# Optimization experiments

Measured on AMD Instinct MI355X. Metric: run time of the kernel, lower is better.

Reference implementation:

```python
import jax, jax.numpy as jnp
import numpy as np

H = 1024   # hidden_dim
C = 56     # numchars
T = 64     # total_timesteps


def setup_inputs() -> dict:
    key = jax.random.key(0)
    ks = jax.random.split(key, 20)

    def p(k, shape, fan_in):
        # torch default Linear/LSTM init: U(-1/sqrt(fan), 1/sqrt(fan))
        return jax.random.uniform(k, shape, jnp.float32, -1.0, 1.0) / np.float32(np.sqrt(fan_in))

    return {
        "input_sentence": jax.random.normal(ks[0], (T, C), jnp.float32),
        # ErrorUnit.W per layer (top-layer ErrorUnit is never run)
        "W0_w": p(ks[1], (H, C), C), "W0_b": p(ks[2], (H,), C),
        "W1_w": p(ks[3], (H, H), H), "W1_b": p(ks[4], (H,), H),
        "W2_w": p(ks[5], (H, H), H), "W2_b": p(ks[6], (H,), H),
        # LSTM input weights; h0=c0=0 every call so W_hh is inert; b = b_ih + b_hh
        "Wih1": p(ks[7], (4 * H, 2 * H), H), "b1": p(ks[8], (4 * H,), H),
        "Wih2": p(ks[9], (4 * H, 2 * H), H), "b2": p(ks[10], (4 * H,), H),
        "Wih3": p(ks[11], (4 * H, H), H), "b3": p(ks[12], (4 * H,), H),
        # StateUnit.V (reconstruction) per layer >= 1; layer0's V is never used
        "V1_w": p(ks[13], (C, H), H), "V1_b": p(ks[14], (C,), H),
        "V2_w": p(ks[15], (H, H), H), "V2_b": p(ks[16], (H,), H),
        "V3_w": p(ks[17], (H, H), H), "V3_b": p(ks[18], (H,), H),
        "iternumber": 500,
    }


def _lstm_out(x, Wih, b):
    # nn.LSTM(seq=1, batch=1) with zero initial state: f-gate dead, h = o*tanh(i*g)
    z = Wih @ x + b
    i, _, g, o = jnp.split(z, 4)
    return jax.nn.sigmoid(o) * jnp.tanh(jax.nn.sigmoid(i) * jnp.tanh(g))


def reference(input_sentence, W0_w, W0_b, W1_w, W1_b, W2_w, W2_b,
              Wih1, b1, Wih2, b2, Wih3, b3,
              V1_w, V1_b, V2_w, V2_b, V3_w, V3_b, iternumber):
    lam = 1e-4 if iternumber <= 1000 else 1e-2  # lambda1 / lambda2 branch
    h, c = W0_w.shape

    def step(carry, x_t):
        # TD1, TD2: previous-timestep TD errors (fed to LSTM inputs)
        # recon1..3: previous-timestep reconstructions from the layer above
        TD1, TD2, recon1, recon2, recon3, loss = carry
        # layer 0: state is clamped to the input char
        nTD0 = x_t - recon1                        # [C]
        BU0 = W0_w @ nTD0 + W0_b                   # [H]
        loss = loss + jnp.sum(jnp.abs(nTD0))       # * lam**0
        # layer 1
        s1 = _lstm_out(jnp.concatenate([BU0, TD1]), Wih1, b1)
        nrecon1 = V1_w @ s1 + V1_b                 # [C]
        nTD1 = s1 - recon2
        BU1 = W1_w @ nTD1 + W1_b
        loss = loss + jnp.sum(jnp.abs(nTD1)) * lam
        # layer 2
        s2 = _lstm_out(jnp.concatenate([BU1, TD2]), Wih2, b2)
        nrecon2 = V2_w @ s2 + V2_b
        nTD2 = s2 - recon3
        BU2 = W2_w @ nTD2 + W2_b
        loss = loss + jnp.sum(jnp.abs(nTD2)) * (lam ** 2)
        # layer 3 (top): ErrorUnit never runs, its TD_err stays zero -> zero loss term
        s3 = _lstm_out(BU2, Wih3, b3)
        nrecon3 = V3_w @ s3 + V3_b
        return (nTD1, nTD2, nrecon1, nrecon2, nrecon3, loss), None

    z = lambda n: jnp.zeros((n,), jnp.float32)
    init = (z(h), z(h), z(c), z(h), z(h), jnp.float32(0.0))
    carry, _ = jax.lax.scan(step, init, input_sentence)
    return carry[-1]
```

## Files before the change

kernel.cpp:

```cpp
#include <hip/hip_runtime.h>

#define CC 56
#define TT 64
#define GRID 1024
#define NT 256
#define NFLAG 64
#define SS 32
#define FB (GRID * SS)
#define AGENT __HIP_MEMORY_SCOPE_AGENT

#define OFF_FWS   147456
#define OFF_W1BF  262144
#define OFF_W2BF  2359296
#define OFF_PRIV  4456448
#define PRIVB     32768

#define PM2  0
#define PM3  3072
#define PW1R 6144
#define PW2R 9216
#define PV2  12288
#define PV3  13312
#define PV1  14336
#define PA0  15360

#define FS1   0
#define FS2   1024
#define FS3   2048
#define FTD1  3072
#define FTD2  5120
#define FRC1  7168

static __device__ __forceinline__ float wredsum(float v) {
#pragma unroll
  for (int m = 32; m; m >>= 1) v += __shfl_xor(v, m, 64);
  return v;
}
static __device__ __forceinline__ float sigm(float x) { return 1.f / (1.f + __expf(-x)); }
static __device__ __forceinline__ float ftanh(float x) {
  x = fminf(15.f, fmaxf(-15.f, x));
  float e = __expf(2.f * x);
  return (e - 1.f) / (e + 1.f);
}

static __device__ __forceinline__ float2 cld2(const float* p) {
  unsigned long long u = __hip_atomic_load((const unsigned long long*)p, __ATOMIC_RELAXED, AGENT);
  union { unsigned long long u; float2 f; } c; c.u = u; return c.f;
}
static __device__ __forceinline__ float4 cld4(const float* p) {
  float2 a = cld2(p), b = cld2(p + 2);
  return make_float4(a.x, a.y, b.x, b.y);
}
static __device__ __forceinline__ float cld1(const float* p) {
  return __uint_as_float(__hip_atomic_load((const unsigned int*)p, __ATOMIC_RELAXED, AGENT));
}
static __device__ __forceinline__ void cst1(float* p, float v) {
  __hip_atomic_store((unsigned int*)p, __float_as_uint(v), __ATOMIC_RELAXED, AGENT);
}
static __device__ __forceinline__ void cstu2(unsigned* p, unsigned a, unsigned b) {
  unsigned long long u = (unsigned long long)a | ((unsigned long long)b << 32);
  __hip_atomic_store((unsigned long long*)p, u, __ATOMIC_RELAXED, AGENT);
}
static __device__ __forceinline__ int ldi(const int* p) {
  return __hip_atomic_load(p, __ATOMIC_RELAXED, AGENT);
}
static __device__ __forceinline__ void sti(int* p, int v) {
  __hip_atomic_store(p, v, __ATOMIC_RELAXED, AGENT);
}

static __device__ __forceinline__ unsigned bfp(float lo, float hi) {
  unsigned a = __float_as_uint(lo), b = __float_as_uint(hi);
  a = (a + 0x7fffu + ((a >> 16) & 1u)) >> 16;
  b = (b + 0x7fffu + ((b >> 16) & 1u)) >> 16;
  return a | (b << 16);
}
static __device__ __forceinline__ float blo(unsigned u) { return __uint_as_float(u << 16); }
static __device__ __forceinline__ float bhi(unsigned u) { return __uint_as_float(u & 0xffff0000u); }
static __device__ __forceinline__ float bdot2(uint2 w, float4 v) {
  float r = blo(w.x) * v.x;
  r = fmaf(bhi(w.x), v.y, r);
  r = fmaf(blo(w.y), v.z, r);
  r = fmaf(bhi(w.y), v.w, r);
  return r;
}

static __device__ __forceinline__ void warr(int* iws, int g, int b) {
  __syncthreads();
  if (threadIdx.x == 0) sti(iws + SS * b, g);
}
static __device__ __forceinline__ void wwait(int* iws, int g, int b) {
  if (b == 0) {
    const int* p0 = iws + SS * threadIdx.x;
    for (;;) {
      int a0 = ldi(p0), a1 = ldi(p0 + SS * 256), a2 = ldi(p0 + SS * 512), a3 = ldi(p0 + SS * 768);
      if (a0 >= g && a1 >= g && a2 >= g && a3 >= g) break;
      __builtin_amdgcn_s_sleep(1);
    }
    __syncthreads();
    if (threadIdx.x < NFLAG) sti(iws + FB + SS * threadIdx.x, g);
  } else {
    if (threadIdx.x == 0)
      while (ldi(iws + FB + SS * (b & (NFLAG - 1))) < g) __builtin_amdgcn_s_sleep(1);
  }
  __asm__ __volatile__("" ::: "memory");
  __syncthreads();
}

static __device__ __forceinline__ float dotw(const float* a, const float* c, int lane) {
  const float4* a4 = (const float4*)a;
  const float4* c4 = (const float4*)c;
  float acc = 0.f;
#pragma unroll
  for (int j = 0; j < 4; ++j) {
    float4 x = a4[lane * 4 + j], y = c4[lane * 4 + j];
    acc = fmaf(x.x, y.x, fmaf(x.y, y.y, fmaf(x.z, y.z, fmaf(x.w, y.w, acc))));
  }
  return wredsum(acc);
}

__global__ void __launch_bounds__(NT, 4) predcells(
    const float* __restrict__ inp,
    const float* __restrict__ W0w, const float* __restrict__ W0b,
    const float* __restrict__ W1w, const float* __restrict__ W1b,
    const float* __restrict__ W2w, const float* __restrict__ W2b,
    const float* __restrict__ Wi1, const float* __restrict__ b1,
    const float* __restrict__ Wi2, const float* __restrict__ b2,
    const float* __restrict__ Wi3, const float* __restrict__ b3,
    const float* __restrict__ V1w, const float* __restrict__ V1b,
    const float* __restrict__ V2w, const float* __restrict__ V2b,
    const float* __restrict__ V3w, const float* __restrict__ V3b,
    const int* __restrict__ itn,
    float* __restrict__ out, char* ws)
{
  const int tid = threadIdx.x;
  const int lane = tid & 63;
  const int wv = tid >> 6;
  const int b = blockIdx.x;
  const bool hasV1 = (b < CC);

  int* iws = (int*)ws;
  float* fws = (float*)(ws + OFF_FWS);
  unsigned short* w1bf = (unsigned short*)(ws + OFF_W1BF);
  unsigned short* w2bf = (unsigned short*)(ws + OFF_W2BF);
  unsigned short* priv = (unsigned short*)(ws + OFF_PRIV + (size_t)b * PRIVB);

  __shared__ float arow[6][1024];
  __shared__ float psX[6][4], psP[3][4], psA[3];
  __shared__ float cs1[3], cs2[3], cs3[3];

  const int gofs = (wv == 0) ? 0 : ((wv == 1) ? 2048 : 3072);

  {
    float4 r1 = ((const float4*)(W1w + (size_t)b * 1024))[tid];
    cstu2((unsigned*)(w1bf + (size_t)b * 1024 + 4 * tid), bfp(r1.x, r1.y), bfp(r1.z, r1.w));
    float4 r2 = ((const float4*)(W2w + (size_t)b * 1024))[tid];
    cstu2((unsigned*)(w2bf + (size_t)b * 1024 + 4 * tid), bfp(r2.x, r2.y), bfp(r2.z, r2.w));
  }
  warr(iws, 1, b);

  const float lam = (itn[0] <= 1000) ? 1e-4f : 1e-2f;
  const float lam2 = lam * lam;
  const float v1b_b = hasV1 ? V1b[b] : 0.f;
  const float v2b_b = V2b[b];
  const float v3b_b = V3b[b];
  float l0 = 0.f, l1 = 0.f, l2 = 0.f;

  if (wv < 3) {
    float c1v = b1[b + gofs] + dotw(Wi1 + (size_t)(b + gofs) * 2048, W0b, lane);
    float c2v = b2[b + gofs] + dotw(Wi2 + (size_t)(b + gofs) * 2048, W1b, lane);
    float c3v = b3[b + gofs] + dotw(Wi3 + (size_t)(b + gofs) * 1024, W2b, lane);
    if (lane == 0) { cs1[wv] = c1v; cs2[wv] = c2v; cs3[wv] = c3v; }
    if (lane < CC) {
      const float* wr = Wi1 + (size_t)(b + gofs) * 2048;
      float acc = 0.f;
      for (int k = 0; k < 1024; ++k) acc = fmaf(wr[k], W0w[k * CC + lane], acc);
      ((float*)(priv + PA0))[wv * CC + lane] = acc;
    }
    {
      float4 x = ((const float4*)(Wi1 + (size_t)(b + gofs) * 2048 + 1024))[lane];
      ((uint2*)(priv + PW1R + wv * 1024))[lane] = make_uint2(bfp(x.x, x.y), bfp(x.z, x.w));
      float4 y = ((const float4*)(Wi2 + (size_t)(b + gofs) * 2048 + 1024))[lane];
      ((uint2*)(priv + PW2R + wv * 1024))[lane] = make_uint2(bfp(y.x, y.y), bfp(y.z, y.w));
    }
  } else {
#pragma unroll
    for (int j = 0; j < 4; ++j) {
      int i = lane * 4 + j;
      float4 a = ((const float4*)(V2w + (size_t)b * 1024))[i];
      ((uint2*)(priv + PV2))[i] = make_uint2(bfp(a.x, a.y), bfp(a.z, a.w));
      float4 c = ((const float4*)(V3w + (size_t)b * 1024))[i];
      ((uint2*)(priv + PV3))[i] = make_uint2(bfp(c.x, c.y), bfp(c.z, c.w));
      if (hasV1) {
        float4 d = ((const float4*)(V1w + (size_t)b * 1024))[i];
        ((uint2*)(priv + PV1))[i] = make_uint2(bfp(d.x, d.y), bfp(d.z, d.w));
      }
    }
  }
  __syncthreads();
  if (wv < 3) {
    float p = 0.f, ax = 0.f;
    if (lane < CC) {
      float xv = inp[lane];
      p = ((const float*)(priv + PA0))[wv * CC + lane] * xv;
      ax = fabsf(xv);
    }
    p = wredsum(p);
    ax = wredsum(ax);
    if (lane == 0) psA[wv] = p;
    if (b == 0 && wv == 0) l0 += ax;
  }
  __syncthreads();
  if (tid == 0) {
    float s1v = sigm(psA[2] + cs1[2]) * ftanh(sigm(psA[0] + cs1[0]) * ftanh(psA[1] + cs1[1]));
    cst1(fws + FS1 + b, s1v);
    cst1(fws + FTD1 + b, s1v);
    cst1(fws + FS3 + b, 0.f);
    cst1(fws + FTD2 + 1024 + b, 0.f);
  }
  wwait(iws, 1, b);

  {
#pragma unroll
    for (int w = 0; w < 3; ++w) {
      int go = (w == 0) ? 0 : ((w == 1) ? 2048 : 3072);
      ((float4*)arow[w])[tid]     = ((const float4*)(Wi2 + (size_t)(b + go) * 2048))[tid];
      ((float4*)arow[3 + w])[tid] = ((const float4*)(Wi3 + (size_t)(b + go) * 1024))[tid];
    }
    __syncthreads();
    float ac[12];
#pragma unroll
    for (int j = 0; j < 12; ++j) ac[j] = 0.f;
    const uint2* wsrc = (const uint2*)w1bf;
#pragma unroll 4
    for (int k = 0; k < 1024; ++k) {
      uint2 wp = wsrc[k * 256 + tid];
      float f0 = blo(wp.x), f1 = bhi(wp.x), f2 = blo(wp.y), f3 = bhi(wp.y);
      float ai = arow[0][k], ag = arow[1][k], ao = arow[2][k];
      ac[0] = fmaf(ai, f0, ac[0]); ac[1] = fmaf(ai, f1, ac[1]); ac[2] = fmaf(ai, f2, ac[2]); ac[3] = fmaf(ai, f3, ac[3]);
      ac[4] = fmaf(ag, f0, ac[4]); ac[5] = fmaf(ag, f1, ac[5]); ac[6] = fmaf(ag, f2, ac[6]); ac[7] = fmaf(ag, f3, ac[7]);
      ac[8] = fmaf(ao, f0, ac[8]); ac[9] = fmaf(ao, f1, ac[9]); ac[10] = fmaf(ao, f2, ac[10]); ac[11] = fmaf(ao, f3, ac[11]);
    }
#pragma unroll
    for (int w = 0; w < 3; ++w)
      ((uint2*)(priv + PM2 + w * 1024))[tid] =
          make_uint2(bfp(ac[w * 4 + 0], ac[w * 4 + 1]), bfp(ac[w * 4 + 2], ac[w * 4 + 3]));
#pragma unroll
    for (int j = 0; j < 12; ++j) ac[j] = 0.f;
    wsrc = (const uint2*)w2bf;
#pragma unroll 4
    for (int k = 0; k < 1024; ++k) {
      uint2 wp = wsrc[k * 256 + tid];
      float f0 = blo(wp.x), f1 = bhi(wp.x), f2 = blo(wp.y), f3 = bhi(wp.y);
      float ai = arow[3][k], ag = arow[4][k], ao = arow[5][k];
      ac[0] = fmaf(ai, f0, ac[0]); ac[1] = fmaf(ai, f1, ac[1]); ac[2] = fmaf(ai, f2, ac[2]); ac[3] = fmaf(ai, f3, ac[3]);
      ac[4] = fmaf(ag, f0, ac[4]); ac[5] = fmaf(ag, f1, ac[5]); ac[6] = fmaf(ag, f2, ac[6]); ac[7] = fmaf(ag, f3, ac[7]);
      ac[8] = fmaf(ao, f0, ac[8]); ac[9] = fmaf(ao, f1, ac[9]); ac[10] = fmaf(ao, f2, ac[10]); ac[11] = fmaf(ao, f3, ac[11]);
    }
#pragma unroll
    for (int w = 0; w < 3; ++w)
      ((uint2*)(priv + PM3 + w * 1024))[tid] =
          make_uint2(bfp(ac[w * 4 + 0], ac[w * 4 + 1]), bfp(ac[w * 4 + 2], ac[w * 4 + 3]));
  }
  warr(iws, 2, b);

  int g = 2;
  const uint2* pm2 = (const uint2*)(priv + PM2);
  const uint2* pm3 = (const uint2*)(priv + PM3);
  const uint2* pw1r = (const uint2*)(priv + PW1R);
  const uint2* pw2r = (const uint2*)(priv + PW2R);
  const uint2* pv2 = (const uint2*)(priv + PV2);
  const uint2* pv3 = (const uint2*)(priv + PV3);
  const uint2* pv1 = (const uint2*)(priv + PV1);
  const float* a0p = (const float*)(priv + PA0);

  for (int t = 0; t < TT; ++t) {
    const int par = t & 1;
    float* td1cur = fws + FTD1 + par * 1024;
    float* td1nxt = fws + FTD1 + (par ^ 1) * 1024;
    float* td2old = fws + FTD2 + (par ^ 1) * 1024;
    float* td2cur = fws + FTD2 + par * 1024;

    uint2 wm2[3]; wm2[0] = pm2[tid]; wm2[1] = pm2[256 + tid]; wm2[2] = pm2[512 + tid];
    uint2 wv3 = pv3[tid];
    uint2 wv1; if (hasV1) wv1 = pv1[tid];
    {
      float4 v = cld4(td2old + 4 * tid);
      uint2 wr0 = pw2r[tid], wr1 = pw2r[256 + tid], wr2 = pw2r[512 + tid];
      float p0 = wredsum(bdot2(wr0, v));
      float p1 = wredsum(bdot2(wr1, v));
      float p2 = wredsum(bdot2(wr2, v));
      if (lane == 0) { psP[0][wv] = p0; psP[1][wv] = p1; psP[2][wv] = p2; }
    }
    wwait(iws, g, b);
    {
      float4 vtd1 = cld4(td1cur + 4 * tid);
      float4 vs3  = cld4(fws + FS3 + 4 * tid);
      float p0 = wredsum(bdot2(wm2[0], vtd1));
      float p1 = wredsum(bdot2(wm2[1], vtd1));
      float p2 = wredsum(bdot2(wm2[2], vtd1));
      float p3 = wredsum(bdot2(wv3, vs3));
      if (lane == 0) { psX[0][wv] = p0; psX[1][wv] = p1; psX[2][wv] = p2; psX[3][wv] = p3; }
      if (hasV1) {
        float4 vs1 = cld4(fws + FS1 + 4 * tid);
        float pv = wredsum(bdot2(wv1, vs1));
        if (lane == 0) psX[4][wv] = pv;
      }
      if (b == 0) {
        float al = wredsum(fabsf(vtd1.x) + fabsf(vtd1.y) + fabsf(vtd1.z) + fabsf(vtd1.w));
        if (lane == 0) psX[5][wv] = al;
      }
      __syncthreads();
      if (tid == 0) {
        float zi = psX[0][0] + psX[0][1] + psX[0][2] + psX[0][3] + psP[0][0] + psP[0][1] + psP[0][2] + psP[0][3] + cs2[0];
        float zg = psX[1][0] + psX[1][1] + psX[1][2] + psX[1][3] + psP[1][0] + psP[1][1] + psP[1][2] + psP[1][3] + cs2[1];
        float zo = psX[2][0] + psX[2][1] + psX[2][2] + psX[2][3] + psP[2][0] + psP[2][1] + psP[2][2] + psP[2][3] + cs2[2];
        float s2v = sigm(zo) * ftanh(sigm(zi) * ftanh(zg));
        float rc3v = (t == 0) ? 0.f : (psX[3][0] + psX[3][1] + psX[3][2] + psX[3][3] + v3b_b);
        cst1(fws + FS2 + b, s2v);
        cst1(td2cur + b, s2v - rc3v);
        if (hasV1) cst1(fws + FRC1 + b, psX[4][0] + psX[4][1] + psX[4][2] + psX[4][3] + v1b_b);
        if (b == 0) l1 += psX[5][0] + psX[5][1] + psX[5][2] + psX[5][3];
      }
    }
    warr(iws, ++g, b);

    uint2 wm3[3]; wm3[0] = pm3[tid]; wm3[1] = pm3[256 + tid]; wm3[2] = pm3[512 + tid];
    uint2 wv2 = pv2[tid];
    {
      float4 v = cld4(td1cur + 4 * tid);
      uint2 wr0 = pw1r[tid], wr1 = pw1r[256 + tid], wr2 = pw1r[512 + tid];
      float p0 = wredsum(bdot2(wr0, v));
      float p1 = wredsum(bdot2(wr1, v));
      float p2 = wredsum(bdot2(wr2, v));
      if (lane == 0) { psP[0][wv] = p0; psP[1][wv] = p1; psP[2][wv] = p2; }
    }
    wwait(iws, g, b);
    {
      float4 vtd2 = cld4(td2cur + 4 * tid);
      float4 vs2  = cld4(fws + FS2 + 4 * tid);
      float p0 = wredsum(bdot2(wm3[0], vtd2));
      float p1 = wredsum(bdot2(wm3[1], vtd2));
      float p2 = wredsum(bdot2(wm3[2], vtd2));
      float p3 = wredsum(bdot2(wv2, vs2));
      if (lane == 0) { psX[0][wv] = p0; psX[1][wv] = p1; psX[2][wv] = p2; psX[3][wv] = p3; }
      if (b == 0) {
        float al = wredsum(fabsf(vtd2.x) + fabsf(vtd2.y) + fabsf(vtd2.z) + fabsf(vtd2.w));
        if (lane == 0) psX[5][wv] = al;
      }
      if (wv < 3) {
        const int tn = (t < TT - 1) ? (t + 1) : (TT - 1);
        float p = 0.f, ax = 0.f;
        if (lane < CC) {
          float xv = inp[tn * CC + lane];
          float rcv = cld1(fws + FRC1 + lane);
          float nd = xv - rcv;
          p = a0p[wv * CC + lane] * nd;
          ax = fabsf(nd);
        }
        p = wredsum(p);
        ax = wredsum(ax);
        if (lane == 0) psA[wv] = p;
        if (b == 0 && wv == 0 && t < TT - 1) l0 += ax;
      }
      __syncthreads();
      if (tid == 0) {
        float z3i = psX[0][0] + psX[0][1] + psX[0][2] + psX[0][3] + cs3[0];
        float z3g = psX[1][0] + psX[1][1] + psX[1][2] + psX[1][3] + cs3[1];
        float z3o = psX[2][0] + psX[2][1] + psX[2][2] + psX[2][3] + cs3[2];
        cst1(fws + FS3 + b, sigm(z3o) * ftanh(sigm(z3i) * ftanh(z3g)));
        float rc2v = psX[3][0] + psX[3][1] + psX[3][2] + psX[3][3] + v2b_b;
        float z1i = psA[0] + psP[0][0] + psP[0][1] + psP[0][2] + psP[0][3] + cs1[0];
        float z1g = psA[1] + psP[1][0] + psP[1][1] + psP[1][2] + psP[1][3] + cs1[1];
        float z1o = psA[2] + psP[2][0] + psP[2][1] + psP[2][2] + psP[2][3] + cs1[2];
        float s1n = sigm(z1o) * ftanh(sigm(z1i) * ftanh(z1g));
        cst1(fws + FS1 + b, s1n);
        cst1(td1nxt + b, s1n - rc2v);
        if (b == 0) l2 += psX[5][0] + psX[5][1] + psX[5][2] + psX[5][3];
      }
    }
    warr(iws, ++g, b);
  }

  if (b == 0 && tid == 0) out[0] = l0 + lam * l1 + lam2 * l2;
}

extern "C" void kernel_launch(void* const* d_in, const int* in_sizes, int n_in,
                              void* d_out, int out_size, void* d_ws, size_t ws_size,
                              hipStream_t stream) {
  const float* inp = (const float*)d_in[0];
  const float* W0w = (const float*)d_in[1];
  const float* W0b = (const float*)d_in[2];
  const float* W1w = (const float*)d_in[3];
  const float* W1b = (const float*)d_in[4];
  const float* W2w = (const float*)d_in[5];
  const float* W2b = (const float*)d_in[6];
  const float* Wi1 = (const float*)d_in[7];
  const float* b1  = (const float*)d_in[8];
  const float* Wi2 = (const float*)d_in[9];
  const float* b2  = (const float*)d_in[10];
  const float* Wi3 = (const float*)d_in[11];
  const float* b3  = (const float*)d_in[12];
  const float* V1w = (const float*)d_in[13];
  const float* V1b = (const float*)d_in[14];
  const float* V2w = (const float*)d_in[15];
  const float* V2b = (const float*)d_in[16];
  const float* V3w = (const float*)d_in[17];
  const float* V3b = (const float*)d_in[18];
  const int*   itn = (const int*)d_in[19];

  hipLaunchKernelGGL(predcells, dim3(GRID), dim3(NT), 0, stream,
                     inp, W0w, W0b, W1w, W1b, W2w, W2b,
                     Wi1, b1, Wi2, b2, Wi3, b3,
                     V1w, V1b, V2w, V2b, V3w, V3b, itn,
                     (float*)d_out, (char*)d_ws);
}
```

Measured before the change: 1.110 ms.

## Use single-wave blocks and shrink the timestep loop to 256 blocks handling four outputs each

Blocks now have one 64-lane wavefront instead of four. Setup still uses 1024 blocks, and the setup GEMM is rewritten so each lane computes 16 columns across all three gates. After setup only 256 blocks stay in the recurrent loop, and each one computes four hidden units. This cuts the number of blocks taking part in each grid-wide barrier and removes the shared-memory partial-sum reductions inside a block. The cost is less parallelism per step, more serial dot-product work per wave, and a barrier that polls 16 or 4 flag slots per lane.

```diff
diff --git a/kernel.cpp b/kernel.cpp
--- a/kernel.cpp
+++ b/kernel.cpp
@@ -3,7 +3,8 @@
 #define CC 56
 #define TT 64
 #define GRID 1024
-#define NT 256
+#define LBLK 256
+#define NT 64
 #define NFLAG 64
 #define SS 32
 #define FB (GRID * SS)
@@ -23,6 +24,7 @@
 #define PV3  13312
 #define PV1  14336
 #define PA0  15360
+#define PCS  15696
 
 #define FS1   0
 #define FS2   1024
@@ -76,30 +78,45 @@
 }
 static __device__ __forceinline__ float blo(unsigned u) { return __uint_as_float(u << 16); }
 static __device__ __forceinline__ float bhi(unsigned u) { return __uint_as_float(u & 0xffff0000u); }
-static __device__ __forceinline__ float bdot2(uint2 w, float4 v) {
-  float r = blo(w.x) * v.x;
-  r = fmaf(bhi(w.x), v.y, r);
-  r = fmaf(blo(w.y), v.z, r);
-  r = fmaf(bhi(w.y), v.w, r);
+static __device__ __forceinline__ float bdot4(uint4 w, float4 a, float4 b) {
+  float r =  blo(w.x) * a.x;
+  r = fmaf(bhi(w.x), a.y, r);
+  r = fmaf(blo(w.y), a.z, r);
+  r = fmaf(bhi(w.y), a.w, r);
+  r = fmaf(blo(w.z), b.x, r);
+  r = fmaf(bhi(w.z), b.y, r);
+  r = fmaf(blo(w.w), b.z, r);
+  r = fmaf(bhi(w.w), b.w, r);
   return r;
 }
+static __device__ __forceinline__ float asum4(float4 v) {
+  return fabsf(v.x) + fabsf(v.y) + fabsf(v.z) + fabsf(v.w);
+}
+
+#define DOT16(base, qoff, A, B, C, D)                                   \
+  ({ const uint4* _w = (const uint4*)(base);                            \
+     uint4 _qa = _w[(qoff) + 2 * lane];                                 \
+     uint4 _qb = _w[(qoff) + 2 * lane + 1];                             \
+     wredsum(bdot4(_qa, A, B) + bdot4(_qb, C, D)); })
 
 static __device__ __forceinline__ void warr(int* iws, int g, int b) {
   __syncthreads();
   if (threadIdx.x == 0) sti(iws + SS * b, g);
 }
-static __device__ __forceinline__ void wwait(int* iws, int g, int b) {
+static __device__ __forceinline__ void wwait(int* iws, int g, int b, int nsl) {
+  const int lane = threadIdx.x;
   if (b == 0) {
-    const int* p0 = iws + SS * threadIdx.x;
+    const int* p0 = iws + SS * lane * nsl;
     for (;;) {
-      int a0 = ldi(p0), a1 = ldi(p0 + SS * 256), a2 = ldi(p0 + SS * 512), a3 = ldi(p0 + SS * 768);
-      if (a0 >= g && a1 >= g && a2 >= g && a3 >= g) break;
+      int ok = 1;
+      for (int s = 0; s < nsl; ++s) ok &= (ldi(p0 + SS * s) >= g);
+      if (ok) break;
       __builtin_amdgcn_s_sleep(1);
     }
     __syncthreads();
-    if (threadIdx.x < NFLAG) sti(iws + FB + SS * threadIdx.x, g);
+    sti(iws + FB + SS * lane, g);
   } else {
-    if (threadIdx.x == 0)
+    if (lane == 0)
       while (ldi(iws + FB + SS * (b & (NFLAG - 1))) < g) __builtin_amdgcn_s_sleep(1);
   }
   __asm__ __volatile__("" ::: "memory");
@@ -118,7 +135,40 @@
   return wredsum(acc);
 }
 
-__global__ void __launch_bounds__(NT, 4) predcells(
+static __device__ __forceinline__ void gemm48(const uint4* wsrc, const float* r0, const float* r1,
+                                              const float* r2, unsigned short* dst, int lane) {
+  float ac[48];
+#pragma unroll
+  for (int i = 0; i < 48; ++i) ac[i] = 0.f;
+#pragma unroll 2
+  for (int k = 0; k < 1024; ++k) {
+    uint4 qa = wsrc[k * 128 + 2 * lane];
+    uint4 qb = wsrc[k * 128 + 2 * lane + 1];
+    float fv[16];
+    fv[0] = blo(qa.x);  fv[1] = bhi(qa.x);  fv[2] = blo(qa.y);  fv[3] = bhi(qa.y);
+    fv[4] = blo(qa.z);  fv[5] = bhi(qa.z);  fv[6] = blo(qa.w);  fv[7] = bhi(qa.w);
+    fv[8] = blo(qb.x);  fv[9] = bhi(qb.x);  fv[10] = blo(qb.y); fv[11] = bhi(qb.y);
+    fv[12] = blo(qb.z); fv[13] = bhi(qb.z); fv[14] = blo(qb.w); fv[15] = bhi(qb.w);
+    float ai = r0[k], ag = r1[k], ao = r2[k];
+#pragma unroll
+    for (int c = 0; c < 16; ++c) {
+      ac[c]      = fmaf(ai, fv[c], ac[c]);
+      ac[16 + c] = fmaf(ag, fv[c], ac[16 + c]);
+      ac[32 + c] = fmaf(ao, fv[c], ac[32 + c]);
+    }
+  }
+#pragma unroll
+  for (int gg = 0; gg < 3; ++gg) {
+    unsigned* d = (unsigned*)(dst + gg * 1024);
+#pragma unroll
+    for (int u = 0; u < 4; ++u)
+      cstu2(d + 8 * lane + 2 * u,
+            bfp(ac[gg * 16 + 4 * u], ac[gg * 16 + 4 * u + 1]),
+            bfp(ac[gg * 16 + 4 * u + 2], ac[gg * 16 + 4 * u + 3]));
+  }
+}
+
+__global__ void __launch_bounds__(NT, 1) predcells(
     const float* __restrict__ inp,
     const float* __restrict__ W0w, const float* __restrict__ W0b,
     const float* __restrict__ W1w, const float* __restrict__ W1b,
@@ -132,11 +182,8 @@
     const int* __restrict__ itn,
     float* __restrict__ out, char* ws)
 {
-  const int tid = threadIdx.x;
-  const int lane = tid & 63;
-  const int wv = tid >> 6;
+  const int lane = threadIdx.x;
   const int b = blockIdx.x;
-  const bool hasV1 = (b < CC);
 
   int* iws = (int*)ws;
   float* fws = (float*)(ws + OFF_FWS);
@@ -145,133 +192,148 @@
   unsigned short* priv = (unsigned short*)(ws + OFF_PRIV + (size_t)b * PRIVB);
 
   __shared__ float arow[6][1024];
-  __shared__ float psX[6][4], psP[3][4], psA[3];
-  __shared__ float cs1[3], cs2[3], cs3[3];
-
-  const int gofs = (wv == 0) ? 0 : ((wv == 1) ? 2048 : 3072);
-
-  {
-    float4 r1 = ((const float4*)(W1w + (size_t)b * 1024))[tid];
-    cstu2((unsigned*)(w1bf + (size_t)b * 1024 + 4 * tid), bfp(r1.x, r1.y), bfp(r1.z, r1.w));
-    float4 r2 = ((const float4*)(W2w + (size_t)b * 1024))[tid];
-    cstu2((unsigned*)(w2bf + (size_t)b * 1024 + 4 * tid), bfp(r2.x, r2.y), bfp(r2.z, r2.w));
-  }
-  warr(iws, 1, b);
 
   const float lam = (itn[0] <= 1000) ? 1e-4f : 1e-2f;
   const float lam2 = lam * lam;
-  const float v1b_b = hasV1 ? V1b[b] : 0.f;
-  const float v2b_b = V2b[b];
-  const float v3b_b = V3b[b];
   float l0 = 0.f, l1 = 0.f, l2 = 0.f;
 
-  if (wv < 3) {
-    float c1v = b1[b + gofs] + dotw(Wi1 + (size_t)(b + gofs) * 2048, W0b, lane);
-    float c2v = b2[b + gofs] + dotw(Wi2 + (size_t)(b + gofs) * 2048, W1b, lane);
-    float c3v = b3[b + gofs] + dotw(Wi3 + (size_t)(b + gofs) * 1024, W2b, lane);
-    if (lane == 0) { cs1[wv] = c1v; cs2[wv] = c2v; cs3[wv] = c3v; }
+  {
+    const float4* r1 = (const float4*)(W1w + (size_t)b * 1024);
+    const float4* r2 = (const float4*)(W2w + (size_t)b * 1024);
+    unsigned* d1 = (unsigned*)(w1bf + (size_t)b * 1024);
+    unsigned* d2 = (unsigned*)(w2bf + (size_t)b * 1024);
+#pragma unroll
+    for (int u = 0; u < 4; ++u) {
+      float4 a = r1[lane * 4 + u];
+      cstu2(d1 + 2 * (lane * 4 + u), bfp(a.x, a.y), bfp(a.z, a.w));
+      float4 c = r2[lane * 4 + u];
+      cstu2(d2 + 2 * (lane * 4 + u), bfp(c.x, c.y), bfp(c.z, c.w));
+    }
+  }
+  warr(iws, 1, b);
+
+  float c1r[3], c2r[3], c3r[3];
+#pragma unroll
+  for (int gg = 0; gg < 3; ++gg) {
+    const int go = (gg == 0) ? 0 : ((gg == 1) ? 2048 : 3072);
+    c1r[gg] = b1[b + go] + dotw(Wi1 + (size_t)(b + go) * 2048, W0b, lane);
+    c2r[gg] = b2[b + go] + dotw(Wi2 + (size_t)(b + go) * 2048, W1b, lane);
+    c3r[gg] = b3[b + go] + dotw(Wi3 + (size_t)(b + go) * 1024, W2b, lane);
+  }
+  {
+    float* pc = (float*)(priv + PCS);
+    if (lane == 0) {
+#pragma unroll
+      for (int gg = 0; gg < 3; ++gg) {
+        cst1(pc + gg, c1r[gg]); cst1(pc + 3 + gg, c2r[gg]); cst1(pc + 6 + gg, c3r[gg]);
+      }
+    }
+  }
+  float A0 = 0.f, A1 = 0.f, A2 = 0.f;
+  {
+    const float* wr0 = Wi1 + (size_t)b * 2048;
+    const float* wr1 = Wi1 + (size_t)(b + 2048) * 2048;
+    const float* wr2 = Wi1 + (size_t)(b + 3072) * 2048;
     if (lane < CC) {
-      const float* wr = Wi1 + (size_t)(b + gofs) * 2048;
-      float acc = 0.f;
-      for (int k = 0; k < 1024; ++k) acc = fmaf(wr[k], W0w[k * CC + lane], acc);
-      ((float*)(priv + PA0))[wv * CC + lane] = acc;
-    }
-    {
-      float4 x = ((const float4*)(Wi1 + (size_t)(b + gofs) * 2048 + 1024))[lane];
-      ((uint2*)(priv + PW1R + wv * 1024))[lane] = make_uint2(bfp(x.x, x.y), bfp(x.z, x.w));
-      float4 y = ((const float4*)(Wi2 + (size_t)(b + gofs) * 2048 + 1024))[lane];
-      ((uint2*)(priv + PW2R + wv * 1024))[lane] = make_uint2(bfp(y.x, y.y), bfp(y.z, y.w));
-    }
-  } else {
-#pragma unroll
-    for (int j = 0; j < 4; ++j) {
-      int i = lane * 4 + j;
-      float4 a = ((const float4*)(V2w + (size_t)b * 1024))[i];
-      ((uint2*)(priv + PV2))[i] = make_uint2(bfp(a.x, a.y), bfp(a.z, a.w));
-      float4 c = ((const float4*)(V3w + (size_t)b * 1024))[i];
-      ((uint2*)(priv + PV3))[i] = make_uint2(bfp(c.x, c.y), bfp(c.z, c.w));
-      if (hasV1) {
-        float4 d = ((const float4*)(V1w + (size_t)b * 1024))[i];
-        ((uint2*)(priv + PV1))[i] = make_uint2(bfp(d.x, d.y), bfp(d.z, d.w));
-      }
-    }
-  }
-  __syncthreads();
-  if (wv < 3) {
-    float p = 0.f, ax = 0.f;
+#pragma unroll 4
+      for (int k = 0; k < 1024; ++k) {
+        float w0 = W0w[k * CC + lane];
+        A0 = fmaf(wr0[k], w0, A0);
+        A1 = fmaf(wr1[k], w0, A1);
+        A2 = fmaf(wr2[k], w0, A2);
+      }
+      float* pa = (float*)(priv + PA0);
+      cst1(pa + 0 * CC + lane, A0);
+      cst1(pa + 1 * CC + lane, A1);
+      cst1(pa + 2 * CC + lane, A2);
+    }
+  }
+#pragma unroll
+  for (int gg = 0; gg < 3; ++gg) {
+    const int go = (gg == 0) ? 0 : ((gg == 1) ? 2048 : 3072);
+    const float4* s1p = (const float4*)(Wi1 + (size_t)(b + go) * 2048 + 1024);
+    const float4* s2p = (const float4*)(Wi2 + (size_t)(b + go) * 2048 + 1024);
+    unsigned* d1 = (unsigned*)(priv + PW1R + gg * 1024);
+    unsigned* d2 = (unsigned*)(priv + PW2R + gg * 1024);
+#pragma unroll
+    for (int u = 0; u < 4; ++u) {
+      float4 x = s1p[lane * 4 + u];
+      cstu2(d1 + 2 * (lane * 4 + u), bfp(x.x, x.y), bfp(x.z, x.w));
+      float4 y = s2p[lane * 4 + u];
+      cstu2(d2 + 2 * (lane * 4 + u), bfp(y.x, y.y), bfp(y.z, y.w));
+    }
+  }
+  {
+    const float4* v2p = (const float4*)(V2w + (size_t)b * 1024);
+    const float4* v3p = (const float4*)(V3w + (size_t)b * 1024);
+    unsigned* d2 = (unsigned*)(priv + PV2);
+    unsigned* d3 = (unsigned*)(priv + PV3);
+#pragma unroll
+    for (int u = 0; u < 4; ++u) {
+      float4 a = v2p[lane * 4 + u]; cstu2(d2 + 2 * (lane * 4 + u), bfp(a.x, a.y), bfp(a.z, a.w));
+      float4 c = v3p[lane * 4 + u]; cstu2(d3 + 2 * (lane * 4 + u), bfp(c.x, c.y), bfp(c.z, c.w));
+    }
+    if (b < CC) {
+      const float4* v1p = (const float4*)(V1w + (size_t)b * 1024);
+      unsigned* d1 = (unsigned*)(priv + PV1);
+#pragma unroll
+      for (int u = 0; u < 4; ++u) {
+        float4 a = v1p[lane * 4 + u]; cstu2(d1 + 2 * (lane * 4 + u), bfp(a.x, a.y), bfp(a.z, a.w));
+      }
+    }
+  }
+  {
+    float p0 = 0.f, p1 = 0.f, p2 = 0.f;
     if (lane < CC) {
       float xv = inp[lane];
-      p = ((const float*)(priv + PA0))[wv * CC + lane] * xv;
-      ax = fabsf(xv);
-    }
-    p = wredsum(p);
-    ax = wredsum(ax);
-    if (lane == 0) psA[wv] = p;
-    if (b == 0 && wv == 0) l0 += ax;
-  }
-  __syncthreads();
-  if (tid == 0) {
-    float s1v = sigm(psA[2] + cs1[2]) * ftanh(sigm(psA[0] + cs1[0]) * ftanh(psA[1] + cs1[1]));
-    cst1(fws + FS1 + b, s1v);
-    cst1(fws + FTD1 + b, s1v);
-    cst1(fws + FS3 + b, 0.f);
-    cst1(fws + FTD2 + 1024 + b, 0.f);
-  }
-  wwait(iws, 1, b);
+      p0 = A0 * xv; p1 = A1 * xv; p2 = A2 * xv;
+    }
+    p0 = wredsum(p0); p1 = wredsum(p1); p2 = wredsum(p2);
+    float s1v = sigm(p2 + c1r[2]) * ftanh(sigm(p0 + c1r[0]) * ftanh(p1 + c1r[1]));
+    if (lane == 0) {
+      cst1(fws + FS1 + b, s1v);
+      cst1(fws + FTD1 + b, s1v);
+      cst1(fws + FS3 + b, 0.f);
+      cst1(fws + FTD2 + 1024 + b, 0.f);
+    }
+    if (b == 0) {
+      float ax = (lane < CC) ? fabsf(inp[lane]) : 0.f;
+      l0 += wredsum(ax);
+    }
+  }
+  wwait(iws, 1, b, 16);
 
   {
 #pragma unroll
     for (int w = 0; w < 3; ++w) {
-      int go = (w == 0) ? 0 : ((w == 1) ? 2048 : 3072);
-      ((float4*)arow[w])[tid]     = ((const float4*)(Wi2 + (size_t)(b + go) * 2048))[tid];
-      ((float4*)arow[3 + w])[tid] = ((const float4*)(Wi3 + (size_t)(b + go) * 1024))[tid];
+      const int go = (w == 0) ? 0 : ((w == 1) ? 2048 : 3072);
+      const float4* a2 = (const float4*)(Wi2 + (size_t)(b + go) * 2048);
+      const float4* a3 = (const float4*)(Wi3 + (size_t)(b + go) * 1024);
+#pragma unroll
+      for (int u = 0; u < 4; ++u) {
+        ((float4*)arow[w])[lane * 4 + u]     = a2[lane * 4 + u];
+        ((float4*)arow[3 + w])[lane * 4 + u] = a3[lane * 4 + u];
+      }
     }
     __syncthreads();
-    float ac[12];
-#pragma unroll
-    for (int j = 0; j < 12; ++j) ac[j] = 0.f;
-    const uint2* wsrc = (const uint2*)w1bf;
-#pragma unroll 4
-    for (int k = 0; k < 1024; ++k) {
-      uint2 wp = wsrc[k * 256 + tid];
-      float f0 = blo(wp.x), f1 = bhi(wp.x), f2 = blo(wp.y), f3 = bhi(wp.y);
-      float ai = arow[0][k], ag = arow[1][k], ao = arow[2][k];
-      ac[0] = fmaf(ai, f0, ac[0]); ac[1] = fmaf(ai, f1, ac[1]); ac[2] = fmaf(ai, f2, ac[2]); ac[3] = fmaf(ai, f3, ac[3]);
-      ac[4] = fmaf(ag, f0, ac[4]); ac[5] = fmaf(ag, f1, ac[5]); ac[6] = fmaf(ag, f2, ac[6]); ac[7] = fmaf(ag, f3, ac[7]);
-      ac[8] = fmaf(ao, f0, ac[8]); ac[9] = fmaf(ao, f1, ac[9]); ac[10] = fmaf(ao, f2, ac[10]); ac[11] = fmaf(ao, f3, ac[11]);
-    }
-#pragma unroll
-    for (int w = 0; w < 3; ++w)
-      ((uint2*)(priv + PM2 + w * 1024))[tid] =
-          make_uint2(bfp(ac[w * 4 + 0], ac[w * 4 + 1]), bfp(ac[w * 4 + 2], ac[w * 4 + 3]));
-#pragma unroll
-    for (int j = 0; j < 12; ++j) ac[j] = 0.f;
-    wsrc = (const uint2*)w2bf;
-#pragma unroll 4
-    for (int k = 0; k < 1024; ++k) {
-      uint2 wp = wsrc[k * 256 + tid];
-      float f0 = blo(wp.x), f1 = bhi(wp.x), f2 = blo(wp.y), f3 = bhi(wp.y);
-      float ai = arow[3][k], ag = arow[4][k], ao = arow[5][k];
-      ac[0] = fmaf(ai, f0, ac[0]); ac[1] = fmaf(ai, f1, ac[1]); ac[2] = fmaf(ai, f2, ac[2]); ac[3] = fmaf(ai, f3, ac[3]);
-      ac[4] = fmaf(ag, f0, ac[4]); ac[5] = fmaf(ag, f1, ac[5]); ac[6] = fmaf(ag, f2, ac[6]); ac[7] = fmaf(ag, f3, ac[7]);
-      ac[8] = fmaf(ao, f0, ac[8]); ac[9] = fmaf(ao, f1, ac[9]); ac[10] = fmaf(ao, f2, ac[10]); ac[11] = fmaf(ao, f3, ac[11]);
-    }
-#pragma unroll
-    for (int w = 0; w < 3; ++w)
-      ((uint2*)(priv + PM3 + w * 1024))[tid] =
-          make_uint2(bfp(ac[w * 4 + 0], ac[w * 4 + 1]), bfp(ac[w * 4 + 2], ac[w * 4 + 3]));
+    gemm48((const uint4*)w1bf, arow[0], arow[1], arow[2], priv + PM2, lane);
+    gemm48((const uint4*)w2bf, arow[3], arow[4], arow[5], priv + PM3, lane);
   }
   warr(iws, 2, b);
 
+  if (b >= LBLK) return;
+
+  unsigned short* prj[4];
+#pragma unroll
+  for (int j = 0; j < 4; ++j)
+    prj[j] = (unsigned short*)(ws + OFF_PRIV + (size_t)(b + LBLK * j) * PRIVB);
+  float v2br[4], v3br[4];
+#pragma unroll
+  for (int j = 0; j < 4; ++j) { v2br[j] = V2b[b + LBLK * j]; v3br[j] = V3b[b + LBLK * j]; }
+  const float v1br = (b < CC) ? V1b[b] : 0.f;
+
+  float cs1r[4][3], cs2r[4][3], cs3r[4][3];
   int g = 2;
-  const uint2* pm2 = (const uint2*)(priv + PM2);
-  const uint2* pm3 = (const uint2*)(priv + PM3);
-  const uint2* pw1r = (const uint2*)(priv + PW1R);
-  const uint2* pw2r = (const uint2*)(priv + PW2R);
-  const uint2* pv2 = (const uint2*)(priv + PV2);
-  const uint2* pv3 = (const uint2*)(priv + PV3);
-  const uint2* pv1 = (const uint2*)(priv + PV1);
-  const float* a0p = (const float*)(priv + PA0);
 
   for (int t = 0; t < TT; ++t) {
     const int par = t & 1;
@@ -280,108 +342,143 @@
     float* td2old = fws + FTD2 + (par ^ 1) * 1024;
     float* td2cur = fws + FTD2 + par * 1024;
 
-    uint2 wm2[3]; wm2[0] = pm2[tid]; wm2[1] = pm2[256 + tid]; wm2[2] = pm2[512 + tid];
-    uint2 wv3 = pv3[tid];
-    uint2 wv1; if (hasV1) wv1 = pv1[tid];
+    float pp[4][3];
+    if (t > 0) {
+      float4 o0 = cld4(td2old + 16 * lane);
+      float4 o1 = cld4(td2old + 16 * lane + 4);
+      float4 o2 = cld4(td2old + 16 * lane + 8);
+      float4 o3 = cld4(td2old + 16 * lane + 12);
+#pragma unroll
+      for (int j = 0; j < 4; ++j) {
+        const unsigned short* wp = prj[j] + PW2R;
+#pragma unroll
+        for (int gg = 0; gg < 3; ++gg) pp[j][gg] = DOT16(wp, gg * 128, o0, o1, o2, o3);
+      }
+    } else {
+#pragma unroll
+      for (int j = 0; j < 4; ++j)
+#pragma unroll
+        for (int gg = 0; gg < 3; ++gg) pp[j][gg] = 0.f;
+    }
+
+    wwait(iws, g, b, (g == 2) ? 16 : 4);
+    if (t == 0) {
+#pragma unroll
+      for (int j = 0; j < 4; ++j) {
+        const float* pc = (const float*)(prj[j] + PCS);
+#pragma unroll
+        for (int gg = 0; gg < 3; ++gg) {
+          cs1r[j][gg] = pc[gg]; cs2r[j][gg] = pc[3 + gg]; cs3r[j][gg] = pc[6 + gg];
+        }
+      }
+    }
+
+    float4 vt0 = cld4(td1cur + 16 * lane);
+    float4 vt1 = cld4(td1cur + 16 * lane + 4);
+    float4 vt2 = cld4(td1cur + 16 * lane + 8);
+    float4 vt3 = cld4(td1cur + 16 * lane + 12);
     {
-      float4 v = cld4(td2old + 4 * tid);
-      uint2 wr0 = pw2r[tid], wr1 = pw2r[256 + tid], wr2 = pw2r[512 + tid];
-      float p0 = wredsum(bdot2(wr0, v));
-      float p1 = wredsum(bdot2(wr1, v));
-      float p2 = wredsum(bdot2(wr2, v));
-      if (lane == 0) { psP[0][wv] = p0; psP[1][wv] = p1; psP[2][wv] = p2; }
-    }
-    wwait(iws, g, b);
+      float4 s30 = cld4(fws + FS3 + 16 * lane);
+      float4 s31 = cld4(fws + FS3 + 16 * lane + 4);
+      float4 s32 = cld4(fws + FS3 + 16 * lane + 8);
+      float4 s33 = cld4(fws + FS3 + 16 * lane + 12);
+      float xz[4][3], xv3[4];
+#pragma unroll
+      for (int j = 0; j < 4; ++j) {
+        const unsigned short* pm = prj[j] + PM2;
+#pragma unroll
+        for (int gg = 0; gg < 3; ++gg) xz[j][gg] = DOT16(pm, gg * 128, vt0, vt1, vt2, vt3);
+        xv3[j] = DOT16(prj[j] + PV3, 0, s30, s31, s32, s33);
+      }
+      float xv1 = 0.f;
+      if (b < CC) {
+        float4 u0 = cld4(fws + FS1 + 16 * lane);
+        float4 u1 = cld4(fws + FS1 + 16 * lane + 4);
+        float4 u2 = cld4(fws + FS1 + 16 * lane + 8);
+        float4 u3 = cld4(fws + FS1 + 16 * lane + 12);
+        xv1 = DOT16(priv + PV1, 0, u0, u1, u2, u3);
+      }
+      if (b == 0)
+        l1 += wredsum(asum4(vt0) + asum4(vt1) + asum4(vt2) + asum4(vt3));
+#pragma unroll
+      for (int j = 0; j < 4; ++j) {
+        float zi = xz[j][0] + pp[j][0] + cs2r[j][0];
+        float zg = xz[j][1] + pp[j][1] + cs2r[j][1];
+        float zo = xz[j][2] + pp[j][2] + cs2r[j][2];
+        float s2v = sigm(zo) * ftanh(sigm(zi) * ftanh(zg));
+        float rc3v = (t == 0) ? 0.f : (xv3[j] + v3br[j]);
+        if (lane == 0) {
+          cst1(fws + FS2 + b + LBLK * j, s2v);
+          cst1(td2cur + b + LBLK * j, s2v - rc3v);
+        }
+      }
+      if (b < CC && lane == 0) cst1(fws + FRC1 + b, xv1 + v1br);
+    }
+    warr(iws, ++g, b);
+
+    float py[4][3];
+#pragma unroll
+    for (int j = 0; j < 4; ++j) {
+      const unsigned short* wp = prj[j] + PW1R;
+#pragma unroll
+      for (int gg = 0; gg < 3; ++gg) py[j][gg] = DOT16(wp, gg * 128, vt0, vt1, vt2, vt3);
+    }
+    wwait(iws, g, b, 4);
+
     {
-      float4 vtd1 = cld4(td1cur + 4 * tid);
-      float4 vs3  = cld4(fws + FS3 + 4 * tid);
-      float p0 = wredsum(bdot2(wm2[0], vtd1));
-      float p1 = wredsum(bdot2(wm2[1], vtd1));
-      float p2 = wredsum(bdot2(wm2[2], vtd1));
-      float p3 = wredsum(bdot2(wv3, vs3));
-      if (lane == 0) { psX[0][wv] = p0; psX[1][wv] = p1; psX[2][wv] = p2; psX[3][wv] = p3; }
-      if (hasV1) {
-        float4 vs1 = cld4(fws + FS1 + 4 * tid);
-        float pv = wredsum(bdot2(wv1, vs1));
-        if (lane == 0) psX[4][wv] = pv;
+      float4 d0 = cld4(td2cur + 16 * lane);
+      float4 d1 = cld4(td2cur + 16 * lane + 4);
+      float4 d2 = cld4(td2cur + 16 * lane + 8);
+      float4 d3 = cld4(td2cur + 16 * lane + 12);
+      float4 e0 = cld4(fws + FS2 + 16 * lane);
+      float4 e1 = cld4(fws + FS2 + 16 * lane + 4);
+      float4 e2 = cld4(fws + FS2 + 16 * lane + 8);
+      float4 e3 = cld4(fws + FS2 + 16 * lane + 12);
+      float nd = 0.f;
+      const int tn = (t < TT - 1) ? (t + 1) : (TT - 1);
+      if (lane < CC) {
+        float xv = inp[tn * CC + lane];
+        float rcv = cld1(fws + FRC1 + lane);
+        nd = xv - rcv;
+      }
+      float yz[4][3], yv2[4], pa[4][3];
+#pragma unroll
+      for (int j = 0; j < 4; ++j) {
+        const unsigned short* pm = prj[j] + PM3;
+#pragma unroll
+        for (int gg = 0; gg < 3; ++gg) yz[j][gg] = DOT16(pm, gg * 128, d0, d1, d2, d3);
+        yv2[j] = DOT16(prj[j] + PV2, 0, e0, e1, e2, e3);
+        const float* pa0 = (const float*)(prj[j] + PA0);
+#pragma unroll
+        for (int gg = 0; gg < 3; ++gg)
+          pa[j][gg] = wredsum((lane < CC) ? pa0[gg * CC + lane] * nd : 0.f);
       }
       if (b == 0) {
-        float al = wredsum(fabsf(vtd1.x) + fabsf(vtd1.y) + fabsf(vtd1.z) + fabsf(vtd1.w));
-        if (lane == 0) psX[5][wv] = al;
-      }
-      __syncthreads();
-      if (tid == 0) {
-        float zi = psX[0][0] + psX[0][1] + psX[0][2] + psX[0][3] + psP[0][0] + psP[0][1] + psP[0][2] + psP[0][3] + cs2[0];
-        float zg = psX[1][0] + psX[1][1] + psX[1][2] + psX[1][3] + psP[1][0] + psP[1][1] + psP[1][2] + psP[1][3] + cs2[1];
-        float zo = psX[2][0] + psX[2][1] + psX[2][2] + psX[2][3] + psP[2][0] + psP[2][1] + psP[2][2] + psP[2][3] + cs2[2];
-        float s2v = sigm(zo) * ftanh(sigm(zi) * ftanh(zg));
-        float rc3v = (t == 0) ? 0.f : (psX[3][0] + psX[3][1] + psX[3][2] + psX[3][3] + v3b_b);
-        cst1(fws + FS2 + b, s2v);
-        cst1(td2cur + b, s2v - rc3v);
-        if (hasV1) cst1(fws + FRC1 + b, psX[4][0] + psX[4][1] + psX[4][2] + psX[4][3] + v1b_b);
-        if (b == 0) l1 += psX[5][0] + psX[5][1] + psX[5][2] + psX[5][3];
+        l2 += wredsum(asum4(d0) + asum4(d1) + asum4(d2) + asum4(d3));
+        if (t < TT - 1) l0 += wredsum((lane < CC) ? fabsf(nd) : 0.f);
+      }
+#pragma unroll
+      for (int j = 0; j < 4; ++j) {
+        float z3i = yz[j][0] + cs3r[j][0];
+        float z3g = yz[j][1] + cs3r[j][1];
+        float z3o = yz[j][2] + cs3r[j][2];
+        float s3v = sigm(z3o) * ftanh(sigm(z3i) * ftanh(z3g));
+        float rc2 = yv2[j] + v2br[j];
+        float z1i = pa[j][0] + py[j][0] + cs1r[j][0];
+        float z1g = pa[j][1] + py[j][1] + cs1r[j][1];
+        float z1o = pa[j][2] + py[j][2] + cs1r[j][2];
+        float s1n = sigm(z1o) * ftanh(sigm(z1i) * ftanh(z1g));
+        if (lane == 0) {
+          cst1(fws + FS3 + b + LBLK * j, s3v);
+          cst1(fws + FS1 + b + LBLK * j, s1n);
+          cst1(td1nxt + b + LBLK * j, s1n - rc2);
+        }
       }
     }
     warr(iws, ++g, b);
-
-    uint2 wm3[3]; wm3[0] = pm3[tid]; wm3[1] = pm3[256 + tid]; wm3[2] = pm3[512 + tid];
-    uint2 wv2 = pv2[tid];
-    {
-      float4 v = cld4(td1cur + 4 * tid);
-      uint2 wr0 = pw1r[tid], wr1 = pw1r[256 + tid], wr2 = pw1r[512 + tid];
-      float p0 = wredsum(bdot2(wr0, v));
-      float p1 = wredsum(bdot2(wr1, v));
-      float p2 = wredsum(bdot2(wr2, v));
-      if (lane == 0) { psP[0][wv] = p0; psP[1][wv] = p1; psP[2][wv] = p2; }
-    }
-    wwait(iws, g, b);
-    {
-      float4 vtd2 = cld4(td2cur + 4 * tid);
-      float4 vs2  = cld4(fws + FS2 + 4 * tid);
-      float p0 = wredsum(bdot2(wm3[0], vtd2));
-      float p1 = wredsum(bdot2(wm3[1], vtd2));
-      float p2 = wredsum(bdot2(wm3[2], vtd2));
-      float p3 = wredsum(bdot2(wv2, vs2));
-      if (lane == 0) { psX[0][wv] = p0; psX[1][wv] = p1; psX[2][wv] = p2; psX[3][wv] = p3; }
-      if (b == 0) {
-        float al = wredsum(fabsf(vtd2.x) + fabsf(vtd2.y) + fabsf(vtd2.z) + fabsf(vtd2.w));
-        if (lane == 0) psX[5][wv] = al;
-      }
-      if (wv < 3) {
-        const int tn = (t < TT - 1) ? (t + 1) : (TT - 1);
-        float p = 0.f, ax = 0.f;
-        if (lane < CC) {
-          float xv = inp[tn * CC + lane];
-          float rcv = cld1(fws + FRC1 + lane);
-          float nd = xv - rcv;
-          p = a0p[wv * CC + lane] * nd;
-          ax = fabsf(nd);
-        }
-        p = wredsum(p);
-        ax = wredsum(ax);
-        if (lane == 0) psA[wv] = p;
-        if (b == 0 && wv == 0 && t < TT - 1) l0 += ax;
-      }
-      __syncthreads();
-      if (tid == 0) {
-        float z3i = psX[0][0] + psX[0][1] + psX[0][2] + psX[0][3] + cs3[0];
-        float z3g = psX[1][0] + psX[1][1] + psX[1][2] + psX[1][3] + cs3[1];
-        float z3o = psX[2][0] + psX[2][1] + psX[2][2] + psX[2][3] + cs3[2];
-        cst1(fws + FS3 + b, sigm(z3o) * ftanh(sigm(z3i) * ftanh(z3g)));
-        float rc2v = psX[3][0] + psX[3][1] + psX[3][2] + psX[3][3] + v2b_b;
-        float z1i = psA[0] + psP[0][0] + psP[0][1] + psP[0][2] + psP[0][3] + cs1[0];
-        float z1g = psA[1] + psP[1][0] + psP[1][1] + psP[1][2] + psP[1][3] + cs1[1];
-        float z1o = psA[2] + psP[2][0] + psP[2][1] + psP[2][2] + psP[2][3] + cs1[2];
-        float s1n = sigm(z1o) * ftanh(sigm(z1i) * ftanh(z1g));
-        cst1(fws + FS1 + b, s1n);
-        cst1(td1nxt + b, s1n - rc2v);
-        if (b == 0) l2 += psX[5][0] + psX[5][1] + psX[5][2] + psX[5][3];
-      }
-    }
-    warr(iws, ++g, b);
-  }
-
-  if (b == 0 && tid == 0) out[0] = l0 + lam * l1 + lam2 * l2;
+  }
+
+  if (b == 0 && lane == 0) out[0] = l0 + lam * l1 + lam2 * l2;
 }
 
 extern "C" void kernel_launch(void* const* d_in, const int* in_sizes, int n_in,
```

New measurement: 2.072 ms. +86.7%, slower.
